# Kernel tuning notes

Hardware: AMD Instinct MI355X
Metric: run time of the kernel (lower is better)

The kernel has to match this reference:

```python
import jax, jax.numpy as jnp
import numpy as np

B, N, F_IN = 32, 512, 16
H, D_HID, D_OUT = 8, 8, 32
ALPHA = 0.2
NEG = -9e15


def setup_inputs() -> dict:
    key = jax.random.key(0)
    ks = jax.random.split(key, 10)
    xv = jax.random.normal(ks[0], (B, N, F_IN), dtype=jnp.float32)
    adj = (jax.random.uniform(ks[1], (B, N, N)) < 0.05).astype(jnp.float32)
    s = 0.1
    W_heads = jax.random.normal(ks[2], (H, F_IN, D_HID), dtype=jnp.float32) * s
    a1 = jax.random.normal(ks[3], (H, D_HID), dtype=jnp.float32) * s
    a2 = jax.random.normal(ks[4], (H, D_HID), dtype=jnp.float32) * s
    W_out = jax.random.normal(ks[5], (H * D_HID, D_OUT), dtype=jnp.float32) * s
    a1_out = jax.random.normal(ks[6], (D_OUT,), dtype=jnp.float32) * s
    a2_out = jax.random.normal(ks[7], (D_OUT,), dtype=jnp.float32) * s
    W_q = jax.random.normal(ks[8], (N * D_OUT, N), dtype=jnp.float32) * s
    b_q = jax.random.normal(ks[9], (N,), dtype=jnp.float32) * s
    return {"xv": xv, "adj": adj, "W_heads": W_heads, "a1": a1, "a2": a2,
            "W_out": W_out, "a1_out": a1_out, "a2_out": a2_out,
            "W_q": W_q, "b_q": b_q}


def _masked_softmax(e, adj_mask):
    # e: [..., N, N]; adj_mask broadcastable bool
    scores = jnp.where(adj_mask, e, NEG)
    return jax.nn.softmax(scores, axis=-1)


def reference(xv, adj, W_heads, a1, a2, W_out, a1_out, a2_out, W_q, b_q):
    mask = adj > 0  # [B, N, N]
    # --- multi-head GAT layer (vectorized over batch and heads) ---
    Wh = jnp.einsum('bnf,hfd->bhnd', xv, W_heads)            # [B,H,N,Dh]
    f1 = jnp.einsum('bhnd,hd->bhn', Wh, a1)                   # a^T[:Dh] . Wh_i
    f2 = jnp.einsum('bhnd,hd->bhn', Wh, a2)                   # a^T[Dh:] . Wh_j
    e = jax.nn.leaky_relu(f1[:, :, :, None] + f2[:, :, None, :], ALPHA)  # [B,H,N,N]
    att = _masked_softmax(e, mask[:, None, :, :])
    h = jnp.einsum('bhnm,bhmd->bhnd', att, Wh)
    h = jax.nn.elu(h)                                         # concat=True heads apply elu
    h_cat = jnp.transpose(h, (0, 2, 1, 3)).reshape(B, N, H * D_HID)  # head-major concat
    # --- output attention layer (concat=False: no internal elu) ---
    Who = jnp.einsum('bnf,fd->bnd', h_cat, W_out)             # [B,N,Do]
    g1 = Who @ a1_out                                         # [B,N]
    g2 = Who @ a2_out
    eo = jax.nn.leaky_relu(g1[:, :, None] + g2[:, None, :], ALPHA)
    att_o = _masked_softmax(eo, mask)
    out = jnp.einsum('bnm,bmd->bnd', att_o, Who)
    out = jax.nn.elu(out)                                     # F.elu applied in forward
    # --- Q head ---
    q = out.reshape(B, N * D_OUT) @ W_q + b_q                 # [B,N]
    return q[..., None]                                       # [B,N,1]
```

## Files before the change

kernel.cpp:

```cpp
#include <hip/hip_runtime.h>
#include <stdint.h>


typedef unsigned long long u64;

__device__ __forceinline__ float eluf(float x) { return x > 0.f ? x : __expf(x) - 1.f; }
__device__ __forceinline__ float lrelu(float x) { return fmaxf(x, 0.2f * x); }

__device__ u64   g_mask[131072];
__device__ float g_hcat[1048576];
__device__ float g_Who[524288];
__device__ float g_g1[16384];
__device__ float g_g2[16384];
__device__ float g_out2[524288];
__device__ float g_partial[2097152];

__global__ __launch_bounds__(256) void k_mask(const float* __restrict__ adj) {
  int wid = blockIdx.x * 4 + (threadIdx.x >> 6);
  int lane = threadIdx.x & 63;
#pragma unroll
  for (int seg = 0; seg < 16; ++seg) {
    int gw = wid * 16 + seg;
    float v = adj[(size_t)(gw >> 3) * 512 + (gw & 7) * 64 + lane];
    u64 bal = __ballot(v > 0.f);
    if (lane == 0) g_mask[gw] = bal;
  }
}

__global__ __launch_bounds__(512) void k_gat(const float* __restrict__ xv,
                                             const float* __restrict__ whd,
                                             const float* __restrict__ a1,
                                             const float* __restrict__ a2) {
  __shared__ float w_s[128];
  __shared__ float a1s[8], a2s[8];
  __shared__ float whp[4104];
  __shared__ float f2s[512];

  int bh = blockIdx.x;
  int b = bh >> 3, h = bh & 7;
  int tid = threadIdx.x;

  const u64* mrow = g_mask + (size_t)b * 4096 + (size_t)tid * 8;
  u64 mreg[8];
#pragma unroll
  for (int w = 0; w < 8; ++w) mreg[w] = mrow[w];

  if (tid < 128) w_s[tid] = whd[h * 128 + tid];
  if (tid < 8) { a1s[tid] = a1[h * 8 + tid]; a2s[tid] = a2[h * 8 + tid]; }
  __syncthreads();

  const float4* xp = (const float4*)(xv + (size_t)(b * 512 + tid) * 16);
  float x[16];
#pragma unroll
  for (int i = 0; i < 4; ++i) {
    float4 v = xp[i];
    x[4 * i] = v.x; x[4 * i + 1] = v.y; x[4 * i + 2] = v.z; x[4 * i + 3] = v.w;
  }
  float wh[8] = {0, 0, 0, 0, 0, 0, 0, 0};
#pragma unroll
  for (int f = 0; f < 16; ++f) {
    float xf = x[f];
#pragma unroll
    for (int d = 0; d < 8; ++d) wh[d] += xf * w_s[f * 8 + d];
  }
  float f1v = 0.f, s2 = 0.f;
#pragma unroll
  for (int d = 0; d < 8; ++d) { f1v += wh[d] * a1s[d]; s2 += wh[d] * a2s[d]; }
  f2s[tid] = s2;
#pragma unroll
  for (int d2 = 0; d2 < 4; ++d2)
    *(float2*)(whp + d2 * 1026 + tid * 2) = make_float2(wh[2 * d2], wh[2 * d2 + 1]);
  __syncthreads();

  float acc[8] = {0, 0, 0, 0, 0, 0, 0, 0};
  float sum = 0.f;
#pragma unroll
  for (int g = 0; g < 4; ++g) {
    u64 m0 = mreg[2 * g], m1 = mreg[2 * g + 1];
    while (m0 | m1) {
      bool use0 = (m0 != 0);
      u64 cur = use0 ? m0 : m1;
      int j = __builtin_ctzll(cur);
      u64 nxt = cur & (cur - 1);
      m0 = use0 ? nxt : m0;
      m1 = use0 ? m1 : nxt;
      int col = g * 128 + (use0 ? 0 : 64) + j;
      float p = __expf(lrelu(f1v + f2s[col]));
      sum += p;
      float2 A = *(const float2*)(whp + col * 2);
      float2 Bv = *(const float2*)(whp + 1026 + col * 2);
      float2 C = *(const float2*)(whp + 2052 + col * 2);
      float2 D = *(const float2*)(whp + 3078 + col * 2);
      acc[0] += p * A.x;  acc[1] += p * A.y;  acc[2] += p * Bv.x; acc[3] += p * Bv.y;
      acc[4] += p * C.x;  acc[5] += p * C.y;  acc[6] += p * D.x;  acc[7] += p * D.y;
    }
  }

  float rs = sum > 0.f ? 1.0f / sum : 0.f;
  float* dst = g_hcat + (size_t)(b * 512 + tid) * 64 + h * 8;
  *(float4*)dst = make_float4(eluf(acc[0] * rs), eluf(acc[1] * rs), eluf(acc[2] * rs), eluf(acc[3] * rs));
  *(float4*)(dst + 4) = make_float4(eluf(acc[4] * rs), eluf(acc[5] * rs), eluf(acc[6] * rs), eluf(acc[7] * rs));
}

__global__ __launch_bounds__(128) void k_who(const float* __restrict__ wout,
                                             const float* __restrict__ a1o,
                                             const float* __restrict__ a2o) {
  __shared__ float wo_s[2048];
  __shared__ float a1s[32], a2s[32];
  int tid = threadIdx.x;
  for (int i = tid; i < 2048; i += 128) wo_s[i] = wout[i];
  if (tid < 32) { a1s[tid] = a1o[tid]; a2s[tid] = a2o[tid]; }
  __syncthreads();

  int idx = blockIdx.x * 128 + tid;
  int g = idx >> 1;
  int db = (idx & 1) * 16;

  const float4* hp = (const float4*)(g_hcat + (size_t)g * 64);
  float acc[16];
#pragma unroll
  for (int d = 0; d < 16; ++d) acc[d] = 0.f;
#pragma unroll
  for (int f4 = 0; f4 < 16; ++f4) {
    float4 h4 = hp[f4];
    float hv[4] = {h4.x, h4.y, h4.z, h4.w};
#pragma unroll
    for (int k = 0; k < 4; ++k) {
      const float* wr = wo_s + (f4 * 4 + k) * 32 + db;
      float hvk = hv[k];
#pragma unroll
      for (int d = 0; d < 16; ++d) acc[d] += hvk * wr[d];
    }
  }
  float s1 = 0.f, s2 = 0.f;
#pragma unroll
  for (int d = 0; d < 16; ++d) { s1 += acc[d] * a1s[db + d]; s2 += acc[d] * a2s[db + d]; }
  s1 += __shfl_xor(s1, 1);
  s2 += __shfl_xor(s2, 1);

  float* wdst = g_Who + (size_t)g * 32 + db;
#pragma unroll
  for (int d4 = 0; d4 < 4; ++d4)
    *(float4*)(wdst + d4 * 4) = make_float4(acc[d4 * 4], acc[d4 * 4 + 1], acc[d4 * 4 + 2], acc[d4 * 4 + 3]);
  if ((idx & 1) == 0) { g_g1[g] = s1; g_g2[g] = s2; }
}

__global__ __launch_bounds__(512) void k_att2() {
  __shared__ float whoT[16416];
  __shared__ float g2s[512];

  int b = blockIdx.x >> 3;
  int t = blockIdx.x & 7;
  int tid = threadIdx.x;
  int l = tid >> 3;
  int dg = tid & 7;
  int row = t * 64 + l;

  const u64* mrow = g_mask + (size_t)b * 4096 + (size_t)row * 8;
  u64 mreg[8];
#pragma unroll
  for (int w = 0; w < 8; ++w) mreg[w] = mrow[w];
  float g1v = g_g1[(size_t)b * 512 + row];

  for (int i = tid; i < 4096; i += 512) {
    int col = i >> 3, dgi = i & 7;
    float4 v = *(const float4*)(g_Who + (size_t)(b * 512 + col) * 32 + dgi * 4);
    whoT[(dgi * 4 + 0) * 513 + col] = v.x;
    whoT[(dgi * 4 + 1) * 513 + col] = v.y;
    whoT[(dgi * 4 + 2) * 513 + col] = v.z;
    whoT[(dgi * 4 + 3) * 513 + col] = v.w;
  }
  g2s[tid] = g_g2[(size_t)b * 512 + tid];
  __syncthreads();

  const float* wp0 = whoT + (dg * 4 + 0) * 513;
  const float* wp1 = whoT + (dg * 4 + 1) * 513;
  const float* wp2 = whoT + (dg * 4 + 2) * 513;
  const float* wp3 = whoT + (dg * 4 + 3) * 513;

  float a0 = 0.f, a1v = 0.f, a2v = 0.f, a3 = 0.f, sum = 0.f;
#pragma unroll
  for (int g = 0; g < 4; ++g) {
    u64 m0 = mreg[2 * g], m1 = mreg[2 * g + 1];
    while (m0 | m1) {
      bool use0 = (m0 != 0);
      u64 cur = use0 ? m0 : m1;
      int j = __builtin_ctzll(cur);
      u64 nxt = cur & (cur - 1);
      m0 = use0 ? nxt : m0;
      m1 = use0 ? m1 : nxt;
      int col = g * 128 + (use0 ? 0 : 64) + j;
      float p = __expf(lrelu(g1v + g2s[col]));
      sum += p;
      a0 += p * wp0[col];
      a1v += p * wp1[col];
      a2v += p * wp2[col];
      a3 += p * wp3[col];
    }
  }

  float rs = sum > 0.f ? 1.0f / sum : 0.f;
  *(float4*)(g_out2 + (size_t)(b * 512 + row) * 32 + dg * 4) =
      make_float4(eluf(a0 * rs), eluf(a1v * rs), eluf(a2v * rs), eluf(a3 * rs));
}

__global__ __launch_bounds__(512) void k_qpart(const float* __restrict__ Wq) {
  __shared__ float wqS[16384];
  __shared__ float outS[4608];
  int s = blockIdx.x >> 2;
  int c = blockIdx.x & 3;
  int tid = threadIdx.x;
  int lane = tid & 63;
  int bg = tid >> 6;

  for (int i = tid; i < 4096; i += 512) {
    int kk = i >> 5, n4 = i & 31;
    *(float4*)(wqS + kk * 128 + n4 * 4) =
        *(const float4*)(Wq + (size_t)(s * 128 + kk) * 512 + c * 128 + n4 * 4);
  }
  for (int i = tid; i < 1024; i += 512) {
    int bb = i >> 5, kk4 = (i & 31) * 4;
    float4 v = *(const float4*)(g_out2 + (size_t)bb * 16384 + s * 128 + kk4);
    outS[(kk4 + 0) * 36 + bb] = v.x;
    outS[(kk4 + 1) * 36 + bb] = v.y;
    outS[(kk4 + 2) * 36 + bb] = v.z;
    outS[(kk4 + 3) * 36 + bb] = v.w;
  }
  __syncthreads();

  float2 acc[4];
#pragma unroll
  for (int j = 0; j < 4; ++j) acc[j] = make_float2(0.f, 0.f);

#pragma unroll 8
  for (int kk = 0; kk < 128; ++kk) {
    float2 wv = *(const float2*)(wqS + kk * 128 + lane * 2);
    const float4 o = *(const float4*)(outS + kk * 36 + bg * 4);
    acc[0].x += o.x * wv.x; acc[0].y += o.x * wv.y;
    acc[1].x += o.y * wv.x; acc[1].y += o.y * wv.y;
    acc[2].x += o.z * wv.x; acc[2].y += o.z * wv.y;
    acc[3].x += o.w * wv.x; acc[3].y += o.w * wv.y;
  }
#pragma unroll
  for (int j = 0; j < 4; ++j)
    *(float2*)(g_partial + (size_t)(s * 32 + bg * 4 + j) * 512 + c * 128 + lane * 2) = acc[j];
}

__global__ __launch_bounds__(256) void k_qred(const float* __restrict__ bq,
                                              float* __restrict__ out) {
  __shared__ float red[4][64];
  int tid = threadIdx.x;
  int w = tid >> 6, lane = tid & 63;
  int g = blockIdx.x * 64 + lane;
  int b = g >> 9, np = g & 511;

  float q = 0.f;
#pragma unroll 8
  for (int i = 0; i < 32; ++i) {
    int s = w + i * 4;
    q += g_partial[(size_t)(s * 32 + b) * 512 + np];
  }
  red[w][lane] = q;
  __syncthreads();
  if (w == 0)
    out[g] = bq[np] + red[0][lane] + red[1][lane] + red[2][lane] + red[3][lane];
}

extern "C" void kernel_launch(void* const* d_in, const int* in_sizes, int n_in,
                              void* d_out, int out_size, void* d_ws, size_t ws_size,
                              hipStream_t stream) {
  const float* xv = (const float*)d_in[0];
  const float* adj = (const float*)d_in[1];
  const float* W_heads = (const float*)d_in[2];
  const float* a1 = (const float*)d_in[3];
  const float* a2 = (const float*)d_in[4];
  const float* W_out = (const float*)d_in[5];
  const float* a1_out = (const float*)d_in[6];
  const float* a2_out = (const float*)d_in[7];
  const float* W_q = (const float*)d_in[8];
  const float* b_q = (const float*)d_in[9];

  k_mask<<<2048, 256, 0, stream>>>(adj);
  k_gat<<<256, 512, 0, stream>>>(xv, W_heads, a1, a2);
  k_who<<<256, 128, 0, stream>>>(W_out, a1_out, a2_out);
  k_att2<<<256, 512, 0, stream>>>();
  k_qpart<<<512, 512, 0, stream>>>(W_q);
  k_qred<<<256, 256, 0, stream>>>(b_q, (float*)d_out);
}
```

Baseline: 170.3 us.

## Split GAT rows across two blocks and fuse Q reduction via atomics

The first-layer attention kernel now launches two blocks per (batch, head). Each row's 8 output dims are split between two threads, which doubles parallelism and halves per-thread accumulator and shared-memory loads, at the cost of each block recomputing Wh for all nodes. The separate partial-sum buffer and reduction kernel are removed. The output is seeded with the bias inside the mask kernel, and the Q-head GEMM blocks atomically add their partials directly into it. This drops a large global write/read and one launch, but adds atomic contention and makes the summation order nondeterministic.

```diff
diff --git a/kernel.cpp b/kernel.cpp
--- a/kernel.cpp
+++ b/kernel.cpp
@@ -13,11 +13,17 @@
 __device__ float g_g1[16384];
 __device__ float g_g2[16384];
 __device__ float g_out2[524288];
-__device__ float g_partial[2097152];
-
-__global__ __launch_bounds__(256) void k_mask(const float* __restrict__ adj) {
-  int wid = blockIdx.x * 4 + (threadIdx.x >> 6);
-  int lane = threadIdx.x & 63;
+
+__global__ __launch_bounds__(256) void k_mask(const float* __restrict__ adj,
+                                              const float* __restrict__ bq,
+                                              float* __restrict__ out) {
+  int tid = threadIdx.x;
+  if (blockIdx.x < 64) {
+    int g = blockIdx.x * 256 + tid;
+    out[g] = bq[g & 511];
+  }
+  int wid = blockIdx.x * 4 + (tid >> 6);
+  int lane = tid & 63;
 #pragma unroll
   for (int seg = 0; seg < 16; ++seg) {
     int gw = wid * 16 + seg;
@@ -35,12 +41,16 @@
   __shared__ float a1s[8], a2s[8];
   __shared__ float whp[4104];
   __shared__ float f2s[512];
-
-  int bh = blockIdx.x;
+  __shared__ float f1s[512];
+
+  int bh = blockIdx.x >> 1;
+  int half = blockIdx.x & 1;
   int b = bh >> 3, h = bh & 7;
   int tid = threadIdx.x;
-
-  const u64* mrow = g_mask + (size_t)b * 4096 + (size_t)tid * 8;
+  int r = half * 256 + (tid >> 1);
+  int dh = tid & 1;
+
+  const u64* mrow = g_mask + (size_t)b * 4096 + (size_t)r * 8;
   u64 mreg[8];
 #pragma unroll
   for (int w = 0; w < 8; ++w) mreg[w] = mrow[w];
@@ -63,16 +73,20 @@
 #pragma unroll
     for (int d = 0; d < 8; ++d) wh[d] += xf * w_s[f * 8 + d];
   }
-  float f1v = 0.f, s2 = 0.f;
-#pragma unroll
-  for (int d = 0; d < 8; ++d) { f1v += wh[d] * a1s[d]; s2 += wh[d] * a2s[d]; }
+  float s1 = 0.f, s2 = 0.f;
+#pragma unroll
+  for (int d = 0; d < 8; ++d) { s1 += wh[d] * a1s[d]; s2 += wh[d] * a2s[d]; }
+  f1s[tid] = s1;
   f2s[tid] = s2;
 #pragma unroll
   for (int d2 = 0; d2 < 4; ++d2)
     *(float2*)(whp + d2 * 1026 + tid * 2) = make_float2(wh[2 * d2], wh[2 * d2 + 1]);
   __syncthreads();
 
-  float acc[8] = {0, 0, 0, 0, 0, 0, 0, 0};
+  float f1v = f1s[r];
+  const float* wpA = whp + (dh * 2) * 1026;
+  const float* wpB = whp + (dh * 2 + 1) * 1026;
+  float acc[4] = {0, 0, 0, 0};
   float sum = 0.f;
 #pragma unroll
   for (int g = 0; g < 4; ++g) {
@@ -87,19 +101,15 @@
       int col = g * 128 + (use0 ? 0 : 64) + j;
       float p = __expf(lrelu(f1v + f2s[col]));
       sum += p;
-      float2 A = *(const float2*)(whp + col * 2);
-      float2 Bv = *(const float2*)(whp + 1026 + col * 2);
-      float2 C = *(const float2*)(whp + 2052 + col * 2);
-      float2 D = *(const float2*)(whp + 3078 + col * 2);
-      acc[0] += p * A.x;  acc[1] += p * A.y;  acc[2] += p * Bv.x; acc[3] += p * Bv.y;
-      acc[4] += p * C.x;  acc[5] += p * C.y;  acc[6] += p * D.x;  acc[7] += p * D.y;
+      float2 A = *(const float2*)(wpA + col * 2);
+      float2 Bv = *(const float2*)(wpB + col * 2);
+      acc[0] += p * A.x; acc[1] += p * A.y; acc[2] += p * Bv.x; acc[3] += p * Bv.y;
     }
   }
 
   float rs = sum > 0.f ? 1.0f / sum : 0.f;
-  float* dst = g_hcat + (size_t)(b * 512 + tid) * 64 + h * 8;
-  *(float4*)dst = make_float4(eluf(acc[0] * rs), eluf(acc[1] * rs), eluf(acc[2] * rs), eluf(acc[3] * rs));
-  *(float4*)(dst + 4) = make_float4(eluf(acc[4] * rs), eluf(acc[5] * rs), eluf(acc[6] * rs), eluf(acc[7] * rs));
+  *(float4*)(g_hcat + (size_t)(b * 512 + r) * 64 + h * 8 + dh * 4) =
+      make_float4(eluf(acc[0] * rs), eluf(acc[1] * rs), eluf(acc[2] * rs), eluf(acc[3] * rs));
 }
 
 __global__ __launch_bounds__(128) void k_who(const float* __restrict__ wout,
@@ -204,7 +214,8 @@
       make_float4(eluf(a0 * rs), eluf(a1v * rs), eluf(a2v * rs), eluf(a3 * rs));
 }
 
-__global__ __launch_bounds__(512) void k_qpart(const float* __restrict__ Wq) {
+__global__ __launch_bounds__(512) void k_qpart(const float* __restrict__ Wq,
+                                               float* __restrict__ out) {
   __shared__ float wqS[16384];
   __shared__ float outS[4608];
   int s = blockIdx.x >> 2;
@@ -242,28 +253,11 @@
     acc[3].x += o.w * wv.x; acc[3].y += o.w * wv.y;
   }
 #pragma unroll
-  for (int j = 0; j < 4; ++j)
-    *(float2*)(g_partial + (size_t)(s * 32 + bg * 4 + j) * 512 + c * 128 + lane * 2) = acc[j];
-}
-
-__global__ __launch_bounds__(256) void k_qred(const float* __restrict__ bq,
-                                              float* __restrict__ out) {
-  __shared__ float red[4][64];
-  int tid = threadIdx.x;
-  int w = tid >> 6, lane = tid & 63;
-  int g = blockIdx.x * 64 + lane;
-  int b = g >> 9, np = g & 511;
-
-  float q = 0.f;
-#pragma unroll 8
-  for (int i = 0; i < 32; ++i) {
-    int s = w + i * 4;
-    q += g_partial[(size_t)(s * 32 + b) * 512 + np];
-  }
-  red[w][lane] = q;
-  __syncthreads();
-  if (w == 0)
-    out[g] = bq[np] + red[0][lane] + red[1][lane] + red[2][lane] + red[3][lane];
+  for (int j = 0; j < 4; ++j) {
+    float* dst = out + (size_t)(bg * 4 + j) * 512 + c * 128 + lane * 2;
+    atomicAdd(dst, acc[j].x);
+    atomicAdd(dst + 1, acc[j].y);
+  }
 }
 
 extern "C" void kernel_launch(void* const* d_in, const int* in_sizes, int n_in,
@@ -280,10 +274,9 @@
   const float* W_q = (const float*)d_in[8];
   const float* b_q = (const float*)d_in[9];
 
-  k_mask<<<2048, 256, 0, stream>>>(adj);
-  k_gat<<<256, 512, 0, stream>>>(xv, W_heads, a1, a2);
+  k_mask<<<2048, 256, 0, stream>>>(adj, b_q, (float*)d_out);
+  k_gat<<<512, 512, 0, stream>>>(xv, W_heads, a1, a2);
   k_who<<<256, 128, 0, stream>>>(W_out, a1_out, a2_out);
   k_att2<<<256, 512, 0, stream>>>();
-  k_qpart<<<512, 512, 0, stream>>>(W_q);
-  k_qred<<<256, 256, 0, stream>>>(b_q, (float*)d_out);
-}
+  k_qpart<<<512, 512, 0, stream>>>(W_q, (float*)d_out);
+}
```

Result: slower. 176.3 us (+3.5%).
